# Optimization experiments

Hardware: AMD Instinct MI355X
Metric: run time of the kernel (lower is better)

The kernel has to match this reference:

```python
import jax, jax.numpy as jnp
import numpy as np

C_M, C_Z, C_H, H = 64, 128, 32, 8
INF = 1000000.0

def _layernorm(x, w, b, eps=1e-5):
    mu = jnp.mean(x, axis=-1, keepdims=True)
    var = jnp.var(x, axis=-1, keepdims=True)
    return (x - mu) * jax.lax.rsqrt(var + eps) * w + b

def setup_inputs() -> dict:
    key = jax.random.key(0)
    ks = jax.random.split(key, 8)
    B, S, N = 1, 256, 512
    m = jax.random.normal(ks[0], (B, S, N, C_M), dtype=jnp.float32)
    z = jax.random.normal(ks[1], (B, N, N, C_Z), dtype=jnp.float32)
    mask = jnp.ones((B, N, N), dtype=jnp.float32)
    sc = lambda f: 1.0 / np.sqrt(f)
    return {
        "m": m, "z": z, "mask": mask,
        "ln_m_w": jnp.ones((C_M,), jnp.float32), "ln_m_b": jnp.zeros((C_M,), jnp.float32),
        "ln_z_w": jnp.ones((C_Z,), jnp.float32), "ln_z_b": jnp.zeros((C_Z,), jnp.float32),
        "W_m": jax.random.normal(ks[2], (H * C_H, C_M), jnp.float32) * sc(C_M),
        "W_g": jax.random.normal(ks[3], (H * C_H, C_M), jnp.float32) * sc(C_M),
        "W_z": jax.random.normal(ks[4], (H, C_Z), jnp.float32) * sc(C_Z),
        "W_o": jax.random.normal(ks[5], (C_M, H * C_H), jnp.float32) * sc(H * C_H),
    }

def reference(m, z, mask, ln_m_w, ln_m_b, ln_z_w, ln_z_b, W_m, W_g, W_z, W_o):
    B, S, N, _ = m.shape
    m_n = _layernorm(m, ln_m_w, ln_m_b)          # (B,S,N,c_m)
    z_n = _layernorm(z, ln_z_w, ln_z_b)          # (B,N,N,c_z)
    Wm = W_m.reshape(H, C_H, C_M)
    Wg = W_g.reshape(H, C_H, C_M)
    # values per head: (B,H,S,N,c_h)
    v = jnp.einsum("bsnc,hec->bhsne", m_n, Wm)
    # pair bias logits: (B,H,N,N)
    b = jnp.einsum("bijc,hc->bhij", z_n, W_z)
    b = b + (1.0 - mask[:, None]) * (-INF)
    w = jax.nn.softmax(b, axis=-1)               # (B,H,N,N)
    # gate: (B,S,N,H*c_h)
    g = jax.nn.sigmoid(jnp.einsum("bsnc,hec->bsnhe", m_n, Wg)).reshape(B, S, N, H * C_H)
    # weighted average broadcast over S: (B,H,S,N,c_h)
    o = jnp.einsum("bhij,bhsje->bhsie", w, v)
    o = jnp.transpose(o, (0, 2, 3, 1, 4)).reshape(B, S, N, H * C_H)
    return (g * o) @ W_o.T                       # (B,S,N,c_m)
```

## Files before the change

kernel.cpp:

```cpp
#include <hip/hip_runtime.h>

#define HC 256

typedef _Float16 f16x8 __attribute__((ext_vector_type(8)));
typedef float f32x4 __attribute__((ext_vector_type(4)));

union h4u { ushort4 u; _Float16 h[4]; };
union h8u { uint4 u; f16x8 h; };

__device__ __forceinline__ float wave_sum(float v) {
    #pragma unroll
    for (int off = 32; off; off >>= 1) v += __shfl_xor(v, off);
    return v;
}
__device__ __forceinline__ float wave_max(float v) {
    #pragma unroll
    for (int off = 32; off; off >>= 1) v = fmaxf(v, __shfl_xor(v, off));
    return v;
}

__device__ __forceinline__ void async16(_Float16* l, const _Float16* gp) {
    __builtin_amdgcn_global_load_lds(
        (const __attribute__((address_space(1))) void*)gp,
        (__attribute__((address_space(3))) void*)l, 16, 0, 0);
}

__global__ __launch_bounds__(256) void k_vg(
    const float* __restrict__ m, const float* __restrict__ lw,
    const float* __restrict__ lb, const float* __restrict__ Wm,
    const float* __restrict__ Wg, _Float16* __restrict__ vt,
    _Float16* __restrict__ g)
{
    __shared__ __align__(16) _Float16 lds[2 * 128 * 72];
    _Float16* Al = lds;
    _Float16* Bl = lds + 128 * 72;

    int tid  = threadIdx.x;
    int lane = tid & 63;
    int r0 = blockIdx.x * 128;
    bool gate = (blockIdx.y >= 2);
    int c0 = (blockIdx.y & 1) * 128;
    const float* Wp = gate ? Wg : Wm;

    int srow = tid >> 1, skoff = (tid & 1) * 32;
    {
        const float4* mg = (const float4*)(m + (size_t)(r0 + srow) * 64 + skoff);
        float xv[32];
        float s1 = 0.f, s2 = 0.f;
        #pragma unroll
        for (int q = 0; q < 8; q++) {
            float4 f = mg[q];
            xv[q*4+0] = f.x; xv[q*4+1] = f.y; xv[q*4+2] = f.z; xv[q*4+3] = f.w;
            s1 += f.x + f.y + f.z + f.w;
            s2 += f.x*f.x + f.y*f.y + f.z*f.z + f.w*f.w;
        }
        s1 += __shfl_xor(s1, 1);
        s2 += __shfl_xor(s2, 1);
        float mu  = s1 * (1.0f / 64.0f);
        float var = s2 * (1.0f / 64.0f) - mu * mu;
        float inv = rsqrtf(var + 1e-5f);

        const float4* wg4 = (const float4*)(Wp + (size_t)(c0 + srow) * 64 + skoff);
        #pragma unroll
        for (int q8 = 0; q8 < 4; q8++) {
            float4 w0 = wg4[q8*2], w1 = wg4[q8*2+1];
            float wf[8] = {w0.x,w0.y,w0.z,w0.w,w1.x,w1.y,w1.z,w1.w};
            f16x8 pa, pb;
            #pragma unroll
            for (int t = 0; t < 8; t++) {
                int c = skoff + q8*8 + t;
                pa[t] = (_Float16)((xv[q8*8+t] - mu) * inv * lw[c] + lb[c]);
                pb[t] = (_Float16)wf[t];
            }
            *(f16x8*)&Al[srow * 72 + skoff + q8*8] = pa;
            *(f16x8*)&Bl[srow * 72 + skoff + q8*8] = pb;
        }
    }
    __syncthreads();

    int wv = tid >> 6;
    int mrow0 = (wv & 1) * 64, ncol0 = (wv >> 1) * 64;
    int quad = lane >> 4, lc = lane & 15;
    const _Float16* afsrc = gate ? Bl : Al;
    const _Float16* bfsrc = gate ? Al : Bl;

    f32x4 acc[4][4];
    #pragma unroll
    for (int mt = 0; mt < 4; mt++)
        #pragma unroll
        for (int nt = 0; nt < 4; nt++) { f32x4 z4 = {0.f,0.f,0.f,0.f}; acc[mt][nt] = z4; }

    #pragma unroll
    for (int kk = 0; kk < 2; kk++) {
        f16x8 af[4], bf[4];
        int kf = kk * 32 + quad * 8;
        #pragma unroll
        for (int mt = 0; mt < 4; mt++)
            af[mt] = *(const f16x8*)&afsrc[(mrow0 + mt * 16 + lc) * 72 + kf];
        #pragma unroll
        for (int nt = 0; nt < 4; nt++)
            bf[nt] = *(const f16x8*)&bfsrc[(ncol0 + nt * 16 + lc) * 72 + kf];
        #pragma unroll
        for (int mt = 0; mt < 4; mt++)
            #pragma unroll
            for (int nt = 0; nt < 4; nt++)
                acc[mt][nt] = __builtin_amdgcn_mfma_f32_16x16x32_f16(af[mt], bf[nt], acc[mt][nt], 0, 0, 0);
    }

    __syncthreads();
    #pragma unroll
    for (int mt = 0; mt < 4; mt++) {
        int yd = mrow0 + mt * 16 + quad * 4;
        #pragma unroll
        for (int nt = 0; nt < 4; nt++) {
            int xd = ncol0 + nt * 16 + lc;
            h4u pk;
            #pragma unroll
            for (int t = 0; t < 4; t++) {
                float v = acc[mt][nt][t];
                if (gate) v = 1.0f / (1.0f + __expf(-v));
                pk.h[t] = (_Float16)v;
            }
            *(ushort4*)&lds[xd * 136 + yd] = pk.u;
        }
    }
    __syncthreads();

    int s_idx = blockIdx.x >> 2;
    int j0 = (blockIdx.x & 3) * 128;
    #pragma unroll
    for (int p = 0; p < 8; p++) {
        int id = p * 256 + tid;
        int xrow = id >> 4;
        int ch = id & 15;
        uint4 val = *(const uint4*)&lds[xrow * 136 + ch * 8];
        if (!gate) {
            int cg = c0 + xrow; int hh = cg >> 5, e = cg & 31;
            *(uint4*)&vt[((size_t)hh * 8192 + s_idx * 32 + e) * 512 + j0 + ch * 8] = val;
        } else {
            *(uint4*)&g[(size_t)(r0 + xrow) * 256 + c0 + ch * 8] = val;
        }
    }
}

__global__ __launch_bounds__(256) void k_bias_softmax(
    const float* __restrict__ z, const float* __restrict__ mask,
    const float* __restrict__ lzw, const float* __restrict__ lzb,
    const float* __restrict__ Wz, _Float16* __restrict__ wout)
{
    __shared__ float WW[8][128];
    __shared__ float LG[8][512];
    __shared__ float Bh[8], Ch[8];
    int tid = threadIdx.x;
    int lane = tid & 63, wv = tid >> 6;

    for (int idx = tid; idx < 1024; idx += 256) {
        int h = idx >> 7, c = idx & 127;
        WW[h][c] = Wz[h * 128 + c] * lzw[c];
    }
    __syncthreads();
    if (tid < 8) {
        float bh = 0.f, ch = 0.f;
        for (int c = 0; c < 128; c++) {
            bh += lzb[c] * Wz[tid * 128 + c];
            ch += WW[tid][c];
        }
        Bh[tid] = bh; Ch[tid] = ch;
    }
    __syncthreads();

    int i = blockIdx.x;
    int sub = tid & 7;
    int jrow = tid >> 3;
    for (int rr = 0; rr < 16; rr++) {
        int j = rr * 32 + jrow;
        const float4* zp = (const float4*)(z + ((size_t)i * 512 + j) * 128 + sub * 16);
        float s1 = 0.f, s2 = 0.f;
        float a[8] = {0.f,0.f,0.f,0.f,0.f,0.f,0.f,0.f};
        #pragma unroll
        for (int q = 0; q < 4; q++) {
            float4 f = zp[q];
            float xs[4] = {f.x, f.y, f.z, f.w};
            #pragma unroll
            for (int t = 0; t < 4; t++) {
                float x = xs[t];
                s1 += x; s2 += x * x;
                #pragma unroll
                for (int h = 0; h < 8; h++) a[h] += x * WW[h][sub * 16 + q * 4 + t];
            }
        }
        #pragma unroll
        for (int off = 1; off < 8; off <<= 1) {
            s1 += __shfl_xor(s1, off);
            s2 += __shfl_xor(s2, off);
            #pragma unroll
            for (int h = 0; h < 8; h++) a[h] += __shfl_xor(a[h], off);
        }
        if (sub == 0) {
            float mu  = s1 * (1.0f / 128.0f);
            float var = s2 * (1.0f / 128.0f) - mu * mu;
            float inv = rsqrtf(var + 1e-5f);
            float mv  = mask[(size_t)i * 512 + j];
            float madd = (1.0f - mv) * (-1000000.0f);
            #pragma unroll
            for (int h = 0; h < 8; h++)
                LG[h][j] = inv * (a[h] - mu * Ch[h]) + Bh[h] + madd;
        }
    }
    __syncthreads();

    #pragma unroll
    for (int hh = 0; hh < 2; hh++) {
        int h = wv * 2 + hh;
        float l[8];
        float mx = -1e30f;
        #pragma unroll
        for (int q = 0; q < 8; q++) {
            l[q] = LG[h][lane + q * 64];
            mx = fmaxf(mx, l[q]);
        }
        mx = wave_max(mx);
        float s = 0.f;
        #pragma unroll
        for (int q = 0; q < 8; q++) {
            l[q] = __expf(l[q] - mx);
            s += l[q];
        }
        s = wave_sum(s);
        float rs = 1.0f / s;
        size_t base = ((size_t)h * 512 + i) * 512;
        #pragma unroll
        for (int q = 0; q < 8; q++)
            wout[base + lane + q * 64] = (_Float16)(l[q] * rs);
    }
}

__global__ __launch_bounds__(256) void k_pav(
    const _Float16* __restrict__ wgt, const _Float16* __restrict__ vt,
    _Float16* __restrict__ g)
{
    __shared__ __align__(16) _Float16 lds[2 * 2 * 128 * 64];
    int h = blockIdx.z;
    int i0 = blockIdx.y * 128;
    int c0 = blockIdx.x * 128;
    const _Float16* A = wgt + (size_t)h * 512 * 512;
    const _Float16* B = vt  + (size_t)h * 8192 * 512;
    int tid = threadIdx.x;
    int lane = tid & 63, wv = tid >> 6;
    int mrow0 = (wv & 1) * 64, ncol0 = (wv >> 1) * 64;
    int quad = lane >> 4, lc = lane & 15;

    int rsub = lane >> 3;
    int csw  = ((lane & 7) ^ rsub) * 8;

    const _Float16* Ag = A + (size_t)(i0 + wv * 32 + rsub) * 512 + csw;
    const _Float16* Bg = B + (size_t)(c0 + wv * 32 + rsub) * 512 + csw;

    f32x4 acc[4][4];
    #pragma unroll
    for (int mt = 0; mt < 4; mt++)
        #pragma unroll
        for (int nt = 0; nt < 4; nt++) { f32x4 z4 = {0.f,0.f,0.f,0.f}; acc[mt][nt] = z4; }

    auto stage = [&](int buf, int kb) {
        _Float16* Als = lds + buf * (2 * 128 * 64);
        _Float16* Bls = Als + 128 * 64;
        #pragma unroll
        for (int t = 0; t < 4; t++) {
            int r = wv * 32 + t * 8;
            async16(&Als[r * 64], Ag + (size_t)(t * 8) * 512 + kb);
            async16(&Bls[r * 64], Bg + (size_t)(t * 8) * 512 + kb);
        }
    };

    stage(0, 0);
    __syncthreads();

    int cur = 0;
    for (int kb = 0; kb < 512; kb += 64) {
        if (kb + 64 < 512) stage(cur ^ 1, kb + 64);

        const _Float16* Al = lds + cur * (2 * 128 * 64);
        const _Float16* Bl = Al + 128 * 64;
        #pragma unroll
        for (int kk = 0; kk < 2; kk++) {
            f16x8 af[4], bf[4];
            #pragma unroll
            for (int mt = 0; mt < 4; mt++) {
                int r = mrow0 + mt * 16 + lc;
                af[mt] = *(const f16x8*)&Bl[r * 64 + (((kk * 4 + quad) ^ (r & 7)) << 3)];
            }
            #pragma unroll
            for (int nt = 0; nt < 4; nt++) {
                int r = ncol0 + nt * 16 + lc;
                bf[nt] = *(const f16x8*)&Al[r * 64 + (((kk * 4 + quad) ^ (r & 7)) << 3)];
            }
            #pragma unroll
            for (int mt = 0; mt < 4; mt++)
                #pragma unroll
                for (int nt = 0; nt < 4; nt++)
                    acc[mt][nt] = __builtin_amdgcn_mfma_f32_16x16x32_f16(af[mt], bf[nt], acc[mt][nt], 0, 0, 0);
        }

        __syncthreads();
        cur ^= 1;
    }

    #pragma unroll
    for (int mt = 0; mt < 4; mt++) {
        int yd = mrow0 + mt * 16 + quad * 4;
        #pragma unroll
        for (int nt = 0; nt < 4; nt++) {
            int xd = ncol0 + nt * 16 + lc;
            h4u pk;
            #pragma unroll
            for (int t = 0; t < 4; t++) pk.h[t] = (_Float16)acc[mt][nt][t];
            *(ushort4*)&lds[xd * 136 + yd] = pk.u;
        }
    }
    __syncthreads();

    #pragma unroll
    for (int p = 0; p < 8; p++) {
        int id = p * 256 + tid;
        int il = id >> 4;
        int ch = id & 15;
        int ng = c0 + ch * 8;
        int sj = ng >> 5, e = ng & 31;
        size_t base = ((size_t)sj * 512 + i0 + il) * HC + h * 32 + e;
        h8u ov, gv, res;
        ov.u = *(const uint4*)&lds[il * 136 + ch * 8];
        gv.u = *(const uint4*)&g[base];
        #pragma unroll
        for (int t = 0; t < 8; t++) res.h[t] = (_Float16)((float)ov.h[t] * (float)gv.h[t]);
        *(uint4*)&g[base] = res.u;
    }
}

__global__ __launch_bounds__(256) void k_out(
    const _Float16* __restrict__ og, const float* __restrict__ Wo,
    float* __restrict__ out)
{
    __shared__ __align__(16) char smem[34816];
    _Float16* Blds = (_Float16*)smem;
    float* Tf = (float*)smem;
    int tid = threadIdx.x;
    int lane = tid & 63, wv = tid >> 6;
    int r0 = blockIdx.x * 128;

    {
        const float4* src = (const float4*)(Wo + (size_t)(tid >> 2) * 256 + (tid & 3) * 64);
        #pragma unroll
        for (int q8 = 0; q8 < 8; q8++) {
            float4 w0 = src[q8*2], w1 = src[q8*2+1];
            float wf[8] = {w0.x,w0.y,w0.z,w0.w,w1.x,w1.y,w1.z,w1.w};
            f16x8 p;
            #pragma unroll
            for (int t = 0; t < 8; t++) p[t] = (_Float16)wf[t];
            *(f16x8*)&Blds[(tid >> 2) * 264 + (tid & 3) * 64 + q8 * 8] = p;
        }
    }
    __syncthreads();

    int quad = lane >> 4, lc = lane & 15;
    f32x4 acc[4][2];
    #pragma unroll
    for (int ct = 0; ct < 4; ct++)
        #pragma unroll
        for (int rt = 0; rt < 2; rt++) { f32x4 z4 = {0.f,0.f,0.f,0.f}; acc[ct][rt] = z4; }

    for (int kb = 0; kb < 256; kb += 32) {
        int kf = kb + quad * 8;
        f16x8 bf[2];
        #pragma unroll
        for (int rt = 0; rt < 2; rt++) {
            int row = r0 + wv * 32 + rt * 16 + lc;
            bf[rt] = *(const f16x8*)(og + (size_t)row * HC + kf);
        }
        f16x8 af[4];
        #pragma unroll
        for (int ct = 0; ct < 4; ct++)
            af[ct] = *(const f16x8*)&Blds[(ct * 16 + lc) * 264 + kf];
        #pragma unroll
        for (int ct = 0; ct < 4; ct++)
            #pragma unroll
            for (int rt = 0; rt < 2; rt++)
                acc[ct][rt] = __builtin_amdgcn_mfma_f32_16x16x32_f16(af[ct], bf[rt], acc[ct][rt], 0, 0, 0);
    }

    __syncthreads();
    #pragma unroll
    for (int ct = 0; ct < 4; ct++) {
        int cd = ct * 16 + quad * 4;
        #pragma unroll
        for (int rt = 0; rt < 2; rt++) {
            int rd = wv * 32 + rt * 16 + lc;
            *(f32x4*)&Tf[rd * 68 + cd] = acc[ct][rt];
        }
    }
    __syncthreads();

    #pragma unroll
    for (int p = 0; p < 8; p++) {
        int id = p * 256 + tid;
        int rl = id >> 4;
        int ch = id & 15;
        uint4 v = *(const uint4*)&Tf[rl * 68 + ch * 4];
        *(uint4*)&out[(size_t)(r0 + rl) * 64 + ch * 4] = v;
    }
}

extern "C" void kernel_launch(void* const* d_in, const int* in_sizes, int n_in,
                              void* d_out, int out_size, void* d_ws, size_t ws_size,
                              hipStream_t stream) {
    const float* m    = (const float*)d_in[0];
    const float* z    = (const float*)d_in[1];
    const float* mask = (const float*)d_in[2];
    const float* lnmw = (const float*)d_in[3];
    const float* lnmb = (const float*)d_in[4];
    const float* lnzw = (const float*)d_in[5];
    const float* lnzb = (const float*)d_in[6];
    const float* Wm   = (const float*)d_in[7];
    const float* Wg   = (const float*)d_in[8];
    const float* Wz   = (const float*)d_in[9];
    const float* Wo   = (const float*)d_in[10];
    float* out = (float*)d_out;

    char* ws = (char*)d_ws;
    _Float16* vt = (_Float16*)ws;
    _Float16* g  = (_Float16*)(ws + 67108864);
    _Float16* w  = (_Float16*)d_out;
    (void)in_sizes; (void)n_in; (void)out_size; (void)ws_size;

    k_vg<<<dim3(1024, 4), 256, 0, stream>>>(m, lnmw, lnmb, Wm, Wg, vt, g);
    k_bias_softmax<<<512, 256, 0, stream>>>(z, mask, lnzw, lnzb, Wz, w);
    k_pav<<<dim3(64, 4, 8), 256, 0, stream>>>(w, vt, g);
    k_out<<<1024, 256, 0, stream>>>(g, Wo, out);
}
```

Before: 389.9 us.

## Reuse normalized m tile across all four V/G column tiles per block

```diff
diff --git a/kernel.cpp b/kernel.cpp
--- a/kernel.cpp
+++ b/kernel.cpp
@@ -25,22 +25,29 @@
         (__attribute__((address_space(3))) void*)l, 16, 0, 0);
 }
 
+__global__ __launch_bounds__(256) void k_wcvt(
+    const float* __restrict__ Wm, const float* __restrict__ Wg,
+    _Float16* __restrict__ Wf)
+{
+    int i = (blockIdx.x * 256 + threadIdx.x) * 4;
+    const float* src = (i < 16384) ? (Wm + i) : (Wg + (i - 16384));
+    float4 f = *(const float4*)src;
+    h4u p;
+    p.h[0] = (_Float16)f.x; p.h[1] = (_Float16)f.y;
+    p.h[2] = (_Float16)f.z; p.h[3] = (_Float16)f.w;
+    *(ushort4*)&Wf[i] = p.u;
+}
+
 __global__ __launch_bounds__(256) void k_vg(
     const float* __restrict__ m, const float* __restrict__ lw,
-    const float* __restrict__ lb, const float* __restrict__ Wm,
-    const float* __restrict__ Wg, _Float16* __restrict__ vt,
-    _Float16* __restrict__ g)
+    const float* __restrict__ lb, const _Float16* __restrict__ Wf,
+    _Float16* __restrict__ vt, _Float16* __restrict__ g)
 {
-    __shared__ __align__(16) _Float16 lds[2 * 128 * 72];
-    _Float16* Al = lds;
-    _Float16* Bl = lds + 128 * 72;
-
+    __shared__ __align__(16) _Float16 Al[128 * 72];
+    __shared__ __align__(16) _Float16 T[128 * 136];
     int tid  = threadIdx.x;
     int lane = tid & 63;
     int r0 = blockIdx.x * 128;
-    bool gate = (blockIdx.y >= 2);
-    int c0 = (blockIdx.y & 1) * 128;
-    const float* Wp = gate ? Wg : Wm;
 
     int srow = tid >> 1, skoff = (tid & 1) * 32;
     {
@@ -60,20 +67,15 @@
         float var = s2 * (1.0f / 64.0f) - mu * mu;
         float inv = rsqrtf(var + 1e-5f);
 
-        const float4* wg4 = (const float4*)(Wp + (size_t)(c0 + srow) * 64 + skoff);
         #pragma unroll
         for (int q8 = 0; q8 < 4; q8++) {
-            float4 w0 = wg4[q8*2], w1 = wg4[q8*2+1];
-            float wf[8] = {w0.x,w0.y,w0.z,w0.w,w1.x,w1.y,w1.z,w1.w};
-            f16x8 pa, pb;
+            f16x8 pa;
             #pragma unroll
             for (int t = 0; t < 8; t++) {
                 int c = skoff + q8*8 + t;
                 pa[t] = (_Float16)((xv[q8*8+t] - mu) * inv * lw[c] + lb[c]);
-                pb[t] = (_Float16)wf[t];
             }
             *(f16x8*)&Al[srow * 72 + skoff + q8*8] = pa;
-            *(f16x8*)&Bl[srow * 72 + skoff + q8*8] = pb;
         }
     }
     __syncthreads();
@@ -81,65 +83,79 @@
     int wv = tid >> 6;
     int mrow0 = (wv & 1) * 64, ncol0 = (wv >> 1) * 64;
     int quad = lane >> 4, lc = lane & 15;
-    const _Float16* afsrc = gate ? Bl : Al;
-    const _Float16* bfsrc = gate ? Al : Bl;
-
-    f32x4 acc[4][4];
-    #pragma unroll
-    for (int mt = 0; mt < 4; mt++)
-        #pragma unroll
-        for (int nt = 0; nt < 4; nt++) { f32x4 z4 = {0.f,0.f,0.f,0.f}; acc[mt][nt] = z4; }
-
-    #pragma unroll
-    for (int kk = 0; kk < 2; kk++) {
-        f16x8 af[4], bf[4];
-        int kf = kk * 32 + quad * 8;
-        #pragma unroll
-        for (int mt = 0; mt < 4; mt++)
-            af[mt] = *(const f16x8*)&afsrc[(mrow0 + mt * 16 + lc) * 72 + kf];
-        #pragma unroll
-        for (int nt = 0; nt < 4; nt++)
-            bf[nt] = *(const f16x8*)&bfsrc[(ncol0 + nt * 16 + lc) * 72 + kf];
-        #pragma unroll
-        for (int mt = 0; mt < 4; mt++)
-            #pragma unroll
-            for (int nt = 0; nt < 4; nt++)
-                acc[mt][nt] = __builtin_amdgcn_mfma_f32_16x16x32_f16(af[mt], bf[nt], acc[mt][nt], 0, 0, 0);
-    }
-
-    __syncthreads();
-    #pragma unroll
-    for (int mt = 0; mt < 4; mt++) {
-        int yd = mrow0 + mt * 16 + quad * 4;
-        #pragma unroll
-        for (int nt = 0; nt < 4; nt++) {
-            int xd = ncol0 + nt * 16 + lc;
-            h4u pk;
-            #pragma unroll
-            for (int t = 0; t < 4; t++) {
-                float v = acc[mt][nt][t];
-                if (gate) v = 1.0f / (1.0f + __expf(-v));
-                pk.h[t] = (_Float16)v;
-            }
-            *(ushort4*)&lds[xd * 136 + yd] = pk.u;
-        }
-    }
-    __syncthreads();
-
     int s_idx = blockIdx.x >> 2;
     int j0 = (blockIdx.x & 3) * 128;
-    #pragma unroll
-    for (int p = 0; p < 8; p++) {
-        int id = p * 256 + tid;
-        int xrow = id >> 4;
-        int ch = id & 15;
-        uint4 val = *(const uint4*)&lds[xrow * 136 + ch * 8];
-        if (!gate) {
-            int cg = c0 + xrow; int hh = cg >> 5, e = cg & 31;
-            *(uint4*)&vt[((size_t)hh * 8192 + s_idx * 32 + e) * 512 + j0 + ch * 8] = val;
-        } else {
-            *(uint4*)&g[(size_t)(r0 + xrow) * 256 + c0 + ch * 8] = val;
-        }
+
+    #pragma unroll 1
+    for (int ct = 0; ct < 4; ct++) {
+        bool gate = (ct >= 2);
+        int c0 = (ct & 1) * 128;
+        int wbase = ct * 128;
+
+        f32x4 acc[4][4];
+        #pragma unroll
+        for (int mt = 0; mt < 4; mt++)
+            #pragma unroll
+            for (int nt = 0; nt < 4; nt++) { f32x4 z4 = {0.f,0.f,0.f,0.f}; acc[mt][nt] = z4; }
+
+        #pragma unroll
+        for (int kk = 0; kk < 2; kk++) {
+            f16x8 af[4], bf[4];
+            int kf = kk * 32 + quad * 8;
+            if (!gate) {
+                #pragma unroll
+                for (int mt = 0; mt < 4; mt++)
+                    af[mt] = *(const f16x8*)&Al[(mrow0 + mt * 16 + lc) * 72 + kf];
+                #pragma unroll
+                for (int nt = 0; nt < 4; nt++)
+                    bf[nt] = *(const f16x8*)&Wf[(size_t)(wbase + ncol0 + nt * 16 + lc) * 64 + kf];
+            } else {
+                #pragma unroll
+                for (int mt = 0; mt < 4; mt++)
+                    af[mt] = *(const f16x8*)&Wf[(size_t)(wbase + mrow0 + mt * 16 + lc) * 64 + kf];
+                #pragma unroll
+                for (int nt = 0; nt < 4; nt++)
+                    bf[nt] = *(const f16x8*)&Al[(ncol0 + nt * 16 + lc) * 72 + kf];
+            }
+            #pragma unroll
+            for (int mt = 0; mt < 4; mt++)
+                #pragma unroll
+                for (int nt = 0; nt < 4; nt++)
+                    acc[mt][nt] = __builtin_amdgcn_mfma_f32_16x16x32_f16(af[mt], bf[nt], acc[mt][nt], 0, 0, 0);
+        }
+
+        #pragma unroll
+        for (int mt = 0; mt < 4; mt++) {
+            int yd = mrow0 + mt * 16 + quad * 4;
+            #pragma unroll
+            for (int nt = 0; nt < 4; nt++) {
+                int xd = ncol0 + nt * 16 + lc;
+                h4u pk;
+                #pragma unroll
+                for (int t = 0; t < 4; t++) {
+                    float v = acc[mt][nt][t];
+                    if (gate) v = 1.0f / (1.0f + __expf(-v));
+                    pk.h[t] = (_Float16)v;
+                }
+                *(ushort4*)&T[xd * 136 + yd] = pk.u;
+            }
+        }
+        __syncthreads();
+
+        #pragma unroll
+        for (int p = 0; p < 8; p++) {
+            int id = p * 256 + tid;
+            int xrow = id >> 4;
+            int ch = id & 15;
+            uint4 val = *(const uint4*)&T[xrow * 136 + ch * 8];
+            if (!gate) {
+                int cg = c0 + xrow; int hh = cg >> 5, e = cg & 31;
+                *(uint4*)&vt[((size_t)hh * 8192 + s_idx * 32 + e) * 512 + j0 + ch * 8] = val;
+            } else {
+                *(uint4*)&g[(size_t)(r0 + xrow) * 256 + c0 + ch * 8] = val;
+            }
+        }
+        __syncthreads();
     }
 }
 
@@ -429,10 +445,12 @@
     char* ws = (char*)d_ws;
     _Float16* vt = (_Float16*)ws;
     _Float16* g  = (_Float16*)(ws + 67108864);
-    _Float16* w  = (_Float16*)d_out;
+    _Float16* w   = (_Float16*)d_out;
+    _Float16* Wf  = (_Float16*)((char*)d_out + 8388608);
     (void)in_sizes; (void)n_in; (void)out_size; (void)ws_size;
 
-    k_vg<<<dim3(1024, 4), 256, 0, stream>>>(m, lnmw, lnmb, Wm, Wg, vt, g);
+    k_wcvt<<<32, 256, 0, stream>>>(Wm, Wg, Wf);
+    k_vg<<<1024, 256, 0, stream>>>(m, lnmw, lnmb, Wf, vt, g);
     k_bias_softmax<<<512, 256, 0, stream>>>(z, mask, lnzw, lnzb, Wz, w);
     k_pav<<<dim3(64, 4, 8), 256, 0, stream>>>(w, vt, g);
     k_out<<<1024, 256, 0, stream>>>(g, Wo, out);
```

After: 377.6 us (median of 2 runs). 1.03x faster.
